# Kernel optimization log

Hardware: AMD Instinct MI355X
Metric: run time of the kernel (lower is better)

The kernel has to match this reference:

```python
import jax, jax.numpy as jnp
import numpy as np

B, POMO, N = 64, 200, 1000
EMB, H, D = 128, 8, 16  # head_num * qkv_dim == embedding_dim
SQRT_EMB = 11.313708498984761
CLIP = 10.0
LORA_SCALE = 16.0 / 16  # alpha / rank = 1.0


def setup_inputs() -> dict:
    key = jax.random.key(0)
    ks = jax.random.split(key, 12)
    s = 1.0 / np.sqrt(EMB)
    return {
        "encoded_nodes": jax.random.normal(ks[0], (B, N, EMB), jnp.float32),
        "encoded_q1": jax.random.normal(ks[1], (B, POMO, EMB), jnp.float32),
        "encoded_last_node": jax.random.normal(ks[2], (B, POMO, EMB), jnp.float32),
        "ninf_mask": jnp.zeros((B, POMO, N), jnp.float32),
        "Wq_first": jax.random.normal(ks[3], (H * D, EMB), jnp.float32) * s,
        "Wq_last": jax.random.normal(ks[4], (H * D, EMB), jnp.float32) * s,
        "Wk": jax.random.normal(ks[5], (H * D, EMB), jnp.float32) * s,
        "Wv": jax.random.normal(ks[6], (H * D, EMB), jnp.float32) * s,
        "Wcomb": jax.random.normal(ks[7], (EMB, H * D), jnp.float32) * s,
        "bcomb": jnp.zeros((EMB,), jnp.float32),
        "lora_q_A": jax.random.normal(ks[8], (16, EMB), jnp.float32) * s,
        "lora_q_B": jax.random.normal(ks[9], (H * D, 16), jnp.float32) * 0.01,
        "lora_c_A": jax.random.normal(ks[10], (16, H * D), jnp.float32) * s,
        "lora_c_B": jax.random.normal(ks[11], (EMB, 16), jnp.float32) * 0.01,
    }


def _heads(x):
    # [B, n, H*D] -> [B, H, n, D]
    b, n, _ = x.shape
    return x.reshape(b, n, H, D).transpose(0, 2, 1, 3)


def reference(encoded_nodes, encoded_q1, encoded_last_node, ninf_mask,
              Wq_first, Wq_last, Wk, Wv, Wcomb, bcomb,
              lora_q_A, lora_q_B, lora_c_A, lora_c_B):
    # set_kv
    k = _heads(encoded_nodes @ Wk.T)   # [B,H,N,D]
    v = _heads(encoded_nodes @ Wv.T)   # [B,H,N,D]
    # set_q1
    q_first = _heads(encoded_q1 @ Wq_first.T)  # [B,H,POMO,D]
    # forward: Wq_last + LoRA delta
    q_last_lin = encoded_last_node @ Wq_last.T \
        + ((encoded_last_node @ lora_q_A.T) @ lora_q_B.T) * LORA_SCALE
    q = q_first + _heads(q_last_lin)  # [B,H,POMO,D]
    # masked multi-head attention (rank3 mask broadcast over heads)
    score = jnp.einsum('bhnd,bhmd->bhnm', q, k) / jnp.sqrt(jnp.float32(D))
    score = score + ninf_mask[:, None, :, :]
    weights = jax.nn.softmax(score, axis=3)
    out = jnp.einsum('bhnm,bhmd->bhnd', weights, v)  # [B,H,POMO,D]
    out_concat = out.transpose(0, 2, 1, 3).reshape(encoded_q1.shape[0], -1, H * D)
    # combine + LoRA delta
    mh = out_concat @ Wcomb.T + bcomb \
        + ((out_concat @ lora_c_A.T) @ lora_c_B.T) * LORA_SCALE  # [B,POMO,EMB]
    # single-head scoring against encoder embeddings, tanh clip, mask, softmax
    score2 = jnp.einsum('bne,bme->bnm', mh, encoded_nodes) / SQRT_EMB
    score_masked = CLIP * jnp.tanh(score2) + ninf_mask
    probs = jax.nn.softmax(score_masked, axis=2)  # [B,POMO,N]
    return probs
```

## Files before the change

### kernel.cpp

```cpp
#include <hip/hip_runtime.h>
#include <hip/hip_bf16.h>


typedef _Float16 f16;
typedef _Float16 f16x2 __attribute__((ext_vector_type(2)));
typedef _Float16 f16x4 __attribute__((ext_vector_type(4)));
typedef _Float16 f16x8 __attribute__((ext_vector_type(8)));
typedef __fp16  h4   __attribute__((ext_vector_type(4)));
typedef float   f32x4 __attribute__((ext_vector_type(4)));

#define LORA_SCALE 1.0f

__device__ __forceinline__ f16x2 pk2(f16 a, f16 b){ f16x2 r; r[0]=a; r[1]=b; return r; }

#if __has_builtin(__builtin_amdgcn_fdot2)
__device__ __forceinline__ float fdot2f(f16x2 a, f16x2 b, float c){ return __builtin_amdgcn_fdot2(a, b, c, false); }
#else
__device__ __forceinline__ float fdot2f(f16x2 a, f16x2 b, float c){ return c + (float)a[0]*(float)b[0] + (float)a[1]*(float)b[1]; }
#endif

#if __has_builtin(__builtin_amdgcn_cvt_pkrtz)
__device__ __forceinline__ f16x2 pkrtz(float a, float b){
  return __builtin_bit_cast(f16x2, __builtin_amdgcn_cvt_pkrtz(a, b));
}
#else
__device__ __forceinline__ f16x2 pkrtz(float a, float b){ return pk2((f16)a, (f16)b); }
#endif

__device__ __forceinline__ f32x4 mfma16(f16x4 a, f16x4 b, f32x4 c){
  return __builtin_amdgcn_mfma_f32_16x16x16f16(
      __builtin_bit_cast(h4, a), __builtin_bit_cast(h4, b), c, 0, 0, 0);
}

__device__ __forceinline__ float sumsq16(const f16* p){
  const f16x8* v = (const f16x8*)p;
  f16x8 a = v[0], b = v[1];
  float s = 0.f;
  s = fdot2f(pk2(a[0],a[1]), pk2(a[0],a[1]), s);
  s = fdot2f(pk2(a[2],a[3]), pk2(a[2],a[3]), s);
  s = fdot2f(pk2(a[4],a[5]), pk2(a[4],a[5]), s);
  s = fdot2f(pk2(a[6],a[7]), pk2(a[6],a[7]), s);
  s = fdot2f(pk2(b[0],b[1]), pk2(b[0],b[1]), s);
  s = fdot2f(pk2(b[2],b[3]), pk2(b[2],b[3]), s);
  s = fdot2f(pk2(b[4],b[5]), pk2(b[4],b[5]), s);
  s = fdot2f(pk2(b[6],b[7]), pk2(b[6],b[7]), s);
  return s;
}

__global__ __launch_bounds__(256) void k0_wconv(const float* __restrict__ Wk,
    const float* __restrict__ Wv, f16* __restrict__ WkvF)
{
  const int i = blockIdx.x*256 + threadIdx.x;
  const float4 v = (i < 4096) ? ((const float4*)Wk)[i] : ((const float4*)Wv)[i-4096];
  f16x2 lo = pkrtz(v.x,v.y), hi = pkrtz(v.z,v.w);
  f16x4 o = __builtin_shufflevector(lo, hi, 0, 1, 2, 3);
  *(f16x4*)(WkvF + i*4) = o;
}

#define NSTR 132
#define WSTR 136
__global__ __launch_bounds__(256) void k1_proj(const float* __restrict__ nodes,
    const f16* __restrict__ WkvF,
    f16* __restrict__ nodesF, f16* __restrict__ Kp, f16* __restrict__ Vt)
{
  __shared__ f16 lds[64*NSTR];
  __shared__ f16 wlds[16*WSTR];
  const int tid = threadIdx.x, lane = tid & 63, w = tid >> 6;
  const int b = blockIdx.y;
  const int n0 = blockIdx.x * 64;
  const int rows = min(64, 1000 - n0);
  for (int i = tid; i < rows*32; i += 256) {
    const int r = i >> 5, cq = i & 31;
    float4 v = ((const float4*)(nodes + ((size_t)b*1000 + n0 + r)*128))[cq];
    f16x2 lo = pkrtz(v.x,v.y), hi = pkrtz(v.z,v.w);
    f16x4 o = __builtin_shufflevector(lo, hi, 0, 1, 2, 3);
    *(f16x4*)(lds + r*NSTR + cq*4) = o;
    *(f16x4*)(nodesF + ((size_t)b*1000 + n0 + r)*128 + cq*4) = o;
  }
  __syncthreads();
  const int col = lane & 15, g = lane >> 4, g4 = g*4;
  const int mloc = w*16 + col;
  f16x4 nf[8];
  #pragma unroll
  for (int kk = 0; kk < 8; ++kk)
    nf[kk] = *(const f16x4*)(lds + min(mloc, rows-1)*NSTR + kk*16 + g4);
  const int wr = tid >> 4, wc = tid & 15;
  for (int ct = 0; ct < 16; ++ct) {
    __syncthreads();
    *(f16x8*)(wlds + wr*WSTR + wc*8) =
        *(const f16x8*)(WkvF + (ct*16 + wr)*128 + wc*8);
    __syncthreads();
    f16x4 wf[8];
    #pragma unroll
    for (int kk = 0; kk < 8; ++kk)
      wf[kk] = *(const f16x4*)(wlds + col*WSTR + kk*16 + g4);
    f32x4 acc = {0.f, 0.f, 0.f, 0.f};
    if (ct < 8) {
      #pragma unroll
      for (int kk = 0; kk < 8; ++kk) acc = mfma16(wf[kk], nf[kk], acc);
      if (mloc < rows) {
        const int nn = n0 + mloc;
        f16x4 ov = __builtin_shufflevector(pk2((f16)acc[0],(f16)acc[1]),
                                           pk2((f16)acc[2],(f16)acc[3]), 0,1,2,3);
        *(f16x4*)(Kp + ((size_t)(b*8+ct)*1000 + nn)*16 + g4) = ov;
      }
    } else {
      #pragma unroll
      for (int kk = 0; kk < 8; ++kk) acc = mfma16(nf[kk], wf[kk], acc);
      if (w*16 + g4 + 3 < rows) {
        const int nbase = n0 + w*16 + g4;
        f16x4 ov = __builtin_shufflevector(pk2((f16)acc[0],(f16)acc[1]),
                                           pk2((f16)acc[2],(f16)acc[3]), 0,1,2,3);
        *(f16x4*)(Vt + ((size_t)(b*8+(ct-8))*16 + col)*1000 + nbase) = ov;
      }
    }
  }
}

__global__ __launch_bounds__(256) void k1b_kmax(const f16* __restrict__ Kp,
    float* __restrict__ kmaxA)
{
  __shared__ float wmax[4];
  const int bh = blockIdx.x, tid = threadIdx.x, lane = tid & 63, w = tid >> 6;
  const f16* base = Kp + (size_t)bh*16000;
  float mx = 0.f;
  for (int n = tid; n < 1000; n += 256) mx = fmaxf(mx, sumsq16(base + n*16));
  #pragma unroll
  for (int off = 32; off; off >>= 1) mx = fmaxf(mx, __shfl_xor(mx, off, 64));
  if (lane == 0) wmax[w] = mx;
  __syncthreads();
  if (tid == 0) {
    float m = fmaxf(fmaxf(wmax[0], wmax[1]), fmaxf(wmax[2], wmax[3]));
    kmaxA[bh] = sqrtf(m);
  }
}

__global__ __launch_bounds__(256) void k2_q(const float* __restrict__ q1,
    const float* __restrict__ last, const float* __restrict__ Wqf,
    const float* __restrict__ Wql, const float* __restrict__ lqA,
    const float* __restrict__ lqB, f16* __restrict__ qF)
{
  __shared__ f16 q1r[32*128];
  __shared__ f16 lar[32*128];
  __shared__ float t16[32*16];
  const int tid = threadIdx.x;
  const int row0 = blockIdx.x * 32;
  {
    const float4* s1 = (const float4*)(q1 + (size_t)row0*128);
    const float4* s2 = (const float4*)(last + (size_t)row0*128);
    f16x2* d1 = (f16x2*)q1r; f16x2* d2 = (f16x2*)lar;
    for (int i = tid; i < 32*32; i += 256) {
      float4 v = s1[i];
      d1[2*i] = pkrtz(v.x,v.y); d1[2*i+1] = pkrtz(v.z,v.w);
      float4 u = s2[i];
      d2[2*i] = pkrtz(u.x,u.y); d2[2*i+1] = pkrtz(u.z,u.w);
    }
  }
  __syncthreads();
  for (int idx = tid; idx < 32*16; idx += 256) {
    const int r = idx >> 4, kk = idx & 15;
    const f16x8* lrow = (const f16x8*)(lar + r*128);
    const float* arow = lqA + kk*128;
    float s = 0.f;
    #pragma unroll
    for (int cc = 0; cc < 16; ++cc) {
      f16x8 a = lrow[cc];
      float4 wa = *(const float4*)(arow + cc*8);
      float4 wb = *(const float4*)(arow + cc*8 + 4);
      s = fdot2f(pk2(a[0],a[1]), pkrtz(wa.x,wa.y), s);
      s = fdot2f(pk2(a[2],a[3]), pkrtz(wa.z,wa.w), s);
      s = fdot2f(pk2(a[4],a[5]), pkrtz(wb.x,wb.y), s);
      s = fdot2f(pk2(a[6],a[7]), pkrtz(wb.z,wb.w), s);
    }
    t16[idx] = s;
  }
  __syncthreads();
  const int c = tid & 127, rg = tid >> 7, rb = rg*16;
  float acc[16];
  #pragma unroll
  for (int r = 0; r < 16; ++r) acc[r] = 0.f;
  const float* wfr = Wqf + c*128;
  const float* wlr = Wql + c*128;
  for (int c0 = 0; c0 < 128; c0 += 16) {
    float4 f0 = *(const float4*)(wfr + c0);
    float4 f1 = *(const float4*)(wfr + c0 + 4);
    float4 f2 = *(const float4*)(wfr + c0 + 8);
    float4 f3 = *(const float4*)(wfr + c0 + 12);
    f16x2 wf[8] = { pkrtz(f0.x,f0.y), pkrtz(f0.z,f0.w), pkrtz(f1.x,f1.y), pkrtz(f1.z,f1.w),
                    pkrtz(f2.x,f2.y), pkrtz(f2.z,f2.w), pkrtz(f3.x,f3.y), pkrtz(f3.z,f3.w) };
    float4 g0 = *(const float4*)(wlr + c0);
    float4 g1 = *(const float4*)(wlr + c0 + 4);
    float4 g2 = *(const float4*)(wlr + c0 + 8);
    float4 g3 = *(const float4*)(wlr + c0 + 12);
    f16x2 wl[8] = { pkrtz(g0.x,g0.y), pkrtz(g0.z,g0.w), pkrtz(g1.x,g1.y), pkrtz(g1.z,g1.w),
                    pkrtz(g2.x,g2.y), pkrtz(g2.z,g2.w), pkrtz(g3.x,g3.y), pkrtz(g3.z,g3.w) };
    #pragma unroll
    for (int r = 0; r < 16; ++r) {
      const f16x8* qp = (const f16x8*)(q1r + (rb+r)*128 + c0);
      const f16x8* lp = (const f16x8*)(lar + (rb+r)*128 + c0);
      f16x8 a0 = qp[0], a1 = qp[1], b0 = lp[0], b1 = lp[1];
      float s = acc[r];
      s = fdot2f(pk2(a0[0],a0[1]), wf[0], s);
      s = fdot2f(pk2(a0[2],a0[3]), wf[1], s);
      s = fdot2f(pk2(a0[4],a0[5]), wf[2], s);
      s = fdot2f(pk2(a0[6],a0[7]), wf[3], s);
      s = fdot2f(pk2(a1[0],a1[1]), wf[4], s);
      s = fdot2f(pk2(a1[2],a1[3]), wf[5], s);
      s = fdot2f(pk2(a1[4],a1[5]), wf[6], s);
      s = fdot2f(pk2(a1[6],a1[7]), wf[7], s);
      s = fdot2f(pk2(b0[0],b0[1]), wl[0], s);
      s = fdot2f(pk2(b0[2],b0[3]), wl[1], s);
      s = fdot2f(pk2(b0[4],b0[5]), wl[2], s);
      s = fdot2f(pk2(b0[6],b0[7]), wl[3], s);
      s = fdot2f(pk2(b1[0],b1[1]), wl[4], s);
      s = fdot2f(pk2(b1[2],b1[3]), wl[5], s);
      s = fdot2f(pk2(b1[4],b1[5]), wl[6], s);
      s = fdot2f(pk2(b1[6],b1[7]), wl[7], s);
      acc[r] = s;
    }
  }
  const float* lb = lqB + c*16;
  float lbv[16];
  #pragma unroll
  for (int i = 0; i < 16; i += 4) {
    float4 t = *(const float4*)(lb + i);
    lbv[i] = t.x; lbv[i+1] = t.y; lbv[i+2] = t.z; lbv[i+3] = t.w;
  }
  #pragma unroll
  for (int r = 0; r < 16; ++r) {
    float dl = 0.f;
    #pragma unroll
    for (int kk = 0; kk < 16; ++kk) dl += t16[(rb+r)*16 + kk] * lbv[kk];
    acc[r] += dl * LORA_SCALE;
  }
  const int h = c >> 4, d = c & 15;
  #pragma unroll
  for (int r = 0; r < 16; ++r) {
    const int grow = row0 + rb + r;
    const int b = grow / 200, m = grow % 200;
    qF[(((size_t)b*8 + h)*200 + m)*16 + d] = (f16)acc[r];
  }
}

__global__ __launch_bounds__(256) void k2b_qnorm(const f16* __restrict__ qF,
    float* __restrict__ qnA)
{
  const int idx = blockIdx.x*256 + threadIdx.x;
  qnA[idx] = sqrtf(sumsq16(qF + (size_t)idx*16));
}

#define VSTRL 516
__global__ __launch_bounds__(512) void k3_attn(const f16* __restrict__ Kp,
    const f16* __restrict__ Vt, const f16* __restrict__ qF,
    const float* __restrict__ mask, const float* __restrict__ kmaxA,
    const float* __restrict__ qnA, f16* __restrict__ Opart,
    float* __restrict__ lpart)
{
  extern __shared__ char smem[];
  f16* Kl = (f16*)smem;
  f16* Vl = (f16*)(smem + 16384);
  const int tid = threadIdx.x;
  const int lane = tid & 63, w = tid >> 6;
  const int b = blockIdx.x, h = blockIdx.y, z = blockIdx.z;
  const int bh = b*8 + h;
  {
    const int nl = tid;
    const int n = z*512 + nl;
    f16x4 v0{}, v1{}, v2{}, v3{};
    if (n < 1000) {
      const f16x4* src = (const f16x4*)(Kp + (size_t)bh*16000 + n*16);
      v0 = src[0]; v1 = src[1]; v2 = src[2]; v3 = src[3];
    }
    const int sw = (nl >> 2) & 3;
    f16* dst = Kl + nl*16;
    *(f16x4*)(dst + (0^sw)*4) = v0;
    *(f16x4*)(dst + (1^sw)*4) = v1;
    *(f16x4*)(dst + (2^sw)*4) = v2;
    *(f16x4*)(dst + (3^sw)*4) = v3;
  }
  {
    const int d = tid >> 5, c16 = (tid & 31) * 16;
    const f16* srow = Vt + (size_t)bh*16000 + d*1000;
    f16* drow = Vl + d*VSTRL + c16;
    const int nbase = z*512 + c16;
    if (nbase + 15 < 1000) {
      const f16x4* s4 = (const f16x4*)(srow + nbase);
      *(f16x4*)(drow)    = s4[0];
      *(f16x4*)(drow+4)  = s4[1];
      *(f16x4*)(drow+8)  = s4[2];
      *(f16x4*)(drow+12) = s4[3];
    } else {
      for (int j = 0; j < 16; ++j) drow[j] = (nbase+j < 1000) ? srow[nbase+j] : (f16)0;
    }
  }
  __syncthreads();

  const int col = lane & 15, g = lane >> 4, g4 = g*4;
  const int kqoff = (g ^ (col >> 2)) * 4;
  const f32x4 zero = {0.f, 0.f, 0.f, 0.f};
  const int tA = w, tB = (w + 8 < 13) ? (w + 8) : 12;
  const int mA = tA*16, mB = tB*16;
  const int mqA = min(mA + col, 199), mqB = min(mB + col, 199);
  const f16x4 qfA = *(const f16x4*)(qF + (size_t)bh*3200 + mqA*16 + g4);
  const f16x4 qfB = *(const f16x4*)(qF + (size_t)bh*3200 + mqB*16 + g4);
  const float kmx = kmaxA[bh];
  const float mbA = -kmx * qnA[bh*200 + mqA] * 0.360673760f;
  const float mbB = -kmx * qnA[bh*200 + mqB] * 0.360673760f;
  const float* mpA = mask + ((size_t)b*200 + mqA)*1000 + z*512;
  const float* mpB = mask + ((size_t)b*200 + mqB)*1000 + z*512;

  f32x4 OA = zero, OB = zero;
  float lA0=0.f, lA1=0.f, lA2=0.f, lA3=0.f;
  float lB0=0.f, lB1=0.f, lB2=0.f, lB3=0.f;
  const int NTc = 32 - z*2;
  #pragma unroll 2
  for (int t = 0; t < NTc; ++t) {
    const int nl = t*16;
    const f16x4 kf = *(const f16x4*)(Kl + (nl+col)*16 + kqoff);
    f32x4 sA = mfma16(kf, qfA, zero);
    f32x4 sB = mfma16(kf, qfB, zero);
    const float4 mkA = *(const float4*)(mpA + nl + g4);
    const float4 mkB = *(const float4*)(mpB + nl + g4);
    const float pA0 = exp2f(fmaf(sA[0], 0.360673760f, fmaf(mkA.x, 1.44269504f, mbA)));
    const float pA1 = exp2f(fmaf(sA[1], 0.360673760f, fmaf(mkA.y, 1.44269504f, mbA)));
    const float pA2 = exp2f(fmaf(sA[2], 0.360673760f, fmaf(mkA.z, 1.44269504f, mbA)));
    const float pA3 = exp2f(fmaf(sA[3], 0.360673760f, fmaf(mkA.w, 1.44269504f, mbA)));
    const float pB0 = exp2f(fmaf(sB[0], 0.360673760f, fmaf(mkB.x, 1.44269504f, mbB)));
    const float pB1 = exp2f(fmaf(sB[1], 0.360673760f, fmaf(mkB.y, 1.44269504f, mbB)));
    const float pB2 = exp2f(fmaf(sB[2], 0.360673760f, fmaf(mkB.z, 1.44269504f, mbB)));
    const float pB3 = exp2f(fmaf(sB[3], 0.360673760f, fmaf(mkB.w, 1.44269504f, mbB)));
    lA0 += pA0; lA1 += pA1; lA2 += pA2; lA3 += pA3;
    lB0 += pB0; lB1 += pB1; lB2 += pB2; lB3 += pB3;
    const f16x4 pfA = __builtin_shufflevector(pkrtz(pA0,pA1), pkrtz(pA2,pA3), 0,1,2,3);
    const f16x4 pfB = __builtin_shufflevector(pkrtz(pB0,pB1), pkrtz(pB2,pB3), 0,1,2,3);
    const f16x4 vf = *(const f16x4*)(Vl + col*VSTRL + nl + g4);
    OA = mfma16(vf, pfA, OA);
    OB = mfma16(vf, pfB, OB);
  }
  if (z == 1) {
    const int nl = 480;
    const f16x4 kf = *(const f16x4*)(Kl + (nl+col)*16 + kqoff);
    f32x4 sA = mfma16(kf, qfA, zero);
    f32x4 sB = mfma16(kf, qfB, zero);
    float pA0=0.f,pA1=0.f,pA2=0.f,pA3=0.f, pB0=0.f,pB1=0.f,pB2=0.f,pB3=0.f;
    if (g < 2) {
      const float4 mkA = *(const float4*)(mpA + nl + g4);
      const float4 mkB = *(const float4*)(mpB + nl + g4);
      pA0 = exp2f(fmaf(sA[0], 0.360673760f, fmaf(mkA.x, 1.44269504f, mbA)));
      pA1 = exp2f(fmaf(sA[1], 0.360673760f, fmaf(mkA.y, 1.44269504f, mbA)));
      pA2 = exp2f(fmaf(sA[2], 0.360673760f, fmaf(mkA.z, 1.44269504f, mbA)));
      pA3 = exp2f(fmaf(sA[3], 0.360673760f, fmaf(mkA.w, 1.44269504f, mbA)));
      pB0 = exp2f(fmaf(sB[0], 0.360673760f, fmaf(mkB.x, 1.44269504f, mbB)));
      pB1 = exp2f(fmaf(sB[1], 0.360673760f, fmaf(mkB.y, 1.44269504f, mbB)));
      pB2 = exp2f(fmaf(sB[2], 0.360673760f, fmaf(mkB.z, 1.44269504f, mbB)));
      pB3 = exp2f(fmaf(sB[3], 0.360673760f, fmaf(mkB.w, 1.44269504f, mbB)));
      lA0 += pA0; lA1 += pA1; lA2 += pA2; lA3 += pA3;
      lB0 += pB0; lB1 += pB1; lB2 += pB2; lB3 += pB3;
    }
    const f16x4 pfA = __builtin_shufflevector(pkrtz(pA0,pA1), pkrtz(pA2,pA3), 0,1,2,3);
    const f16x4 pfB = __builtin_shufflevector(pkrtz(pB0,pB1), pkrtz(pB2,pB3), 0,1,2,3);
    const f16x4 vf = *(const f16x4*)(Vl + col*VSTRL + ((g < 2) ? (nl + g4) : 0));
    OA = mfma16(vf, pfA, OA);
    OB = mfma16(vf, pfB, OB);
  }
  float lA = (lA0 + lA1) + (lA2 + lA3);
  float lB = (lB0 + lB1) + (lB2 + lB3);
  lA += __shfl_xor(lA, 16, 64); lA += __shfl_xor(lA, 32, 64);
  lB += __shfl_xor(lB, 16, 64); lB += __shfl_xor(lB, 32, 64);
  const size_t pbase = (size_t)(z*512 + bh)*200;
  if (mA + col < 200) {
    const f16x4 ov = __builtin_shufflevector(pkrtz(OA[0], OA[1]), pkrtz(OA[2], OA[3]), 0,1,2,3);
    *(f16x4*)(Opart + (pbase + mA + col)*16 + g4) = ov;
    if (g == 0) lpart[pbase + mA + col] = lA;
  }
  if (mB + col < 200) {
    const f16x4 ov = __builtin_shufflevector(pkrtz(OB[0], OB[1]), pkrtz(OB[2], OB[3]), 0,1,2,3);
    *(f16x4*)(Opart + (pbase + mB + col)*16 + g4) = ov;
    if (g == 0) lpart[pbase + mB + col] = lB;
  }
}

__global__ __launch_bounds__(256) void k3c_comb(const f16* __restrict__ Opart,
    const float* __restrict__ lpart, f16* __restrict__ ocmh)
{
  const int idx = blockIdx.x*256 + threadIdx.x;
  const int r = idx >> 2, q = idx & 3;
  const f16x4 o0 = *(const f16x4*)(Opart + (size_t)r*16 + q*4);
  const f16x4 o1 = *(const f16x4*)(Opart + ((size_t)102400 + r)*16 + q*4);
  const float l = lpart[r] + lpart[102400 + r];
  const float inv = 1.f / fmaxf(l, 1e-35f);
  const int bh = r / 200, m = r - bh*200;
  const int b = bh >> 3, hh = bh & 7;
  const float v0 = ((float)o0[0] + (float)o1[0]) * inv;
  const float v1 = ((float)o0[1] + (float)o1[1]) * inv;
  const float v2 = ((float)o0[2] + (float)o1[2]) * inv;
  const float v3 = ((float)o0[3] + (float)o1[3]) * inv;
  const f16x4 o = __builtin_shufflevector(pkrtz(v0, v1), pkrtz(v2, v3), 0, 1, 2, 3);
  *(f16x4*)(ocmh + ((size_t)(b*200 + m)*128) + hh*16 + q*4) = o;
}

__global__ __launch_bounds__(256) void k4_comb(const f16* ocF,
    const float* __restrict__ Wc, const float* __restrict__ bc,
    const float* __restrict__ lcA, const float* __restrict__ lcB,
    f16* mhF)
{
  __shared__ f16 ocr[32*128];
  __shared__ float t16[32*16];
  const int tid = threadIdx.x;
  const int row0 = blockIdx.x * 32;
  {
    const f16x8* s1 = (const f16x8*)(ocF + (size_t)row0*128);
    f16x8* d1 = (f16x8*)ocr;
    for (int i = tid; i < 512; i += 256) d1[i] = s1[i];
  }
  __syncthreads();
  for (int idx = tid; idx < 32*16; idx += 256) {
    const int r = idx >> 4, kk = idx & 15;
    const f16x8* lrow = (const f16x8*)(ocr + r*128);
    const float* arow = lcA + kk*128;
    float s = 0.f;
    #pragma unroll
    for (int cc = 0; cc < 16; ++cc) {
      f16x8 a = lrow[cc];
      float4 wa = *(const float4*)(arow + cc*8);
      float4 wb = *(const float4*)(arow + cc*8 + 4);
      s = fdot2f(pk2(a[0],a[1]), pkrtz(wa.x,wa.y), s);
      s = fdot2f(pk2(a[2],a[3]), pkrtz(wa.z,wa.w), s);
      s = fdot2f(pk2(a[4],a[5]), pkrtz(wb.x,wb.y), s);
      s = fdot2f(pk2(a[6],a[7]), pkrtz(wb.z,wb.w), s);
    }
    t16[idx] = s;
  }
  __syncthreads();
  const int c = tid & 127, rg = tid >> 7, rb = rg*16;
  float acc[16];
  const float bias = bc[c];
  #pragma unroll
  for (int r = 0; r < 16; ++r) acc[r] = bias;
  const float* wrow = Wc + c*128;
  for (int c0 = 0; c0 < 128; c0 += 16) {
    float4 w0 = *(const float4*)(wrow + c0);
    float4 w1 = *(const float4*)(wrow + c0 + 4);
    float4 w2 = *(const float4*)(wrow + c0 + 8);
    float4 w3 = *(const float4*)(wrow + c0 + 12);
    f16x2 wv[8] = { pkrtz(w0.x,w0.y), pkrtz(w0.z,w0.w), pkrtz(w1.x,w1.y), pkrtz(w1.z,w1.w),
                    pkrtz(w2.x,w2.y), pkrtz(w2.z,w2.w), pkrtz(w3.x,w3.y), pkrtz(w3.z,w3.w) };
    #pragma unroll
    for (int r = 0; r < 16; ++r) {
      const f16x8* op = (const f16x8*)(ocr + (rb+r)*128 + c0);
      f16x8 a0 = op[0], a1 = op[1];
      float s = acc[r];
      s = fdot2f(pk2(a0[0],a0[1]), wv[0], s);
      s = fdot2f(pk2(a0[2],a0[3]), wv[1], s);
      s = fdot2f(pk2(a0[4],a0[5]), wv[2], s);
      s = fdot2f(pk2(a0[6],a0[7]), wv[3], s);
      s = fdot2f(pk2(a1[0],a1[1]), wv[4], s);
      s = fdot2f(pk2(a1[2],a1[3]), wv[5], s);
      s = fdot2f(pk2(a1[4],a1[5]), wv[6], s);
      s = fdot2f(pk2(a1[6],a1[7]), wv[7], s);
      acc[r] = s;
    }
  }
  const float* lb = lcB + c*16;
  float lbv[16];
  #pragma unroll
  for (int i = 0; i < 16; i += 4) {
    float4 t = *(const float4*)(lb + i);
    lbv[i] = t.x; lbv[i+1] = t.y; lbv[i+2] = t.z; lbv[i+3] = t.w;
  }
  #pragma unroll
  for (int r = 0; r < 16; ++r) {
    float dl = 0.f;
    #pragma unroll
    for (int kk = 0; kk < 16; ++kk) dl += t16[(rb+r)*16 + kk] * lbv[kk];
    acc[r] += dl * LORA_SCALE;
  }
  #pragma unroll
  for (int r = 0; r < 16; ++r) {
    mhF[(size_t)(row0 + rb + r)*128 + c] = (f16)acc[r];
  }
}

__global__ __launch_bounds__(1024) void k5_final(const f16* __restrict__ mhF,
    const f16* __restrict__ nodesF, const float* __restrict__ mask,
    float* __restrict__ out)
{
  __shared__ float sumsA[16][16];
  __shared__ float sumsB[16][16];
  const int tid = threadIdx.x, lane = tid & 63, w = tid >> 6;
  const int b = blockIdx.x, j = blockIdx.y;
  const int col = lane & 15, g = lane >> 4, g4 = g*4;
  const int tmA = 2*j, tmB = min(2*j + 1, 12);
  const int mA = tmA*16 + col, mB = tmB*16 + col;
  const int mqA = min(mA, 199), mqB = min(mB, 199);
  f16x4 bfA[8], bfB[8];
  {
    const f16* a = mhF + (size_t)(b*200 + mqA)*128;
    const f16* bb = mhF + (size_t)(b*200 + mqB)*128;
    #pragma unroll
    for (int kk = 0; kk < 8; ++kk) {
      bfA[kk] = *(const f16x4*)(a + kk*16 + g4);
      bfB[kk] = *(const f16x4*)(bb + kk*16 + g4);
    }
  }
  const float* mrowA = mask + (size_t)(b*200 + mqA)*1000;
  const float* mrowB = mask + (size_t)(b*200 + mqB)*1000;
  const f16* nb = nodesF + (size_t)b*128000;
  f16x4 pfA[4], pfB[4];
  float lsumA = 0.f, lsumB = 0.f;
  #pragma unroll
  for (int i = 0; i < 4; ++i) {
    const int t = w + i*16;
    float pA0 = 0.f, pA1 = 0.f, pA2 = 0.f, pA3 = 0.f;
    float pB0 = 0.f, pB1 = 0.f, pB2 = 0.f, pB3 = 0.f;
    if (t < 63) {
      const int nr = min(t*16 + col, 999);
      const f16* na = nb + nr*128;
      f32x4 accA = {0.f, 0.f, 0.f, 0.f};
      f32x4 accB = {0.f, 0.f, 0.f, 0.f};
      #pragma unroll
      for (int kk = 0; kk < 8; ++kk) {
        f16x4 af = *(const f16x4*)(na + kk*16 + g4);
        accA = mfma16(af, bfA[kk], accA);
        accB = mfma16(af, bfB[kk], accB);
      }
      const int n0 = t*16 + g4;
      float mkvA[4] = {0.f, 0.f, 0.f, 0.f};
      float mkvB[4] = {0.f, 0.f, 0.f, 0.f};
      if (n0 + 3 < 1000) {
        float4 mkA = *(const float4*)(mrowA + n0);
        float4 mkB = *(const float4*)(mrowB + n0);
        mkvA[0] = mkA.x; mkvA[1] = mkA.y; mkvA[2] = mkA.z; mkvA[3] = mkA.w;
        mkvB[0] = mkB.x; mkvB[1] = mkB.y; mkvB[2] = mkB.z; mkvB[3] = mkB.w;
      }
      float pvA[4], pvB[4];
      #pragma unroll
      for (int r = 0; r < 4; ++r) {
        const bool ok = (n0 + r < 1000);
        float xA = accA[r] * 0.08838834764831845f;
        float eA = exp2f(xA * 2.8853900817779268f);
        float thA = 1.f - 2.f/(eA + 1.f);
        float tA0 = exp2f((10.f*thA + mkvA[r]) * 1.44269504f);
        pvA[r] = ok ? tA0 : 0.f;
        lsumA += pvA[r];
        float xB = accB[r] * 0.08838834764831845f;
        float eB = exp2f(xB * 2.8853900817779268f);
        float thB = 1.f - 2.f/(eB + 1.f);
        float tB0 = exp2f((10.f*thB + mkvB[r]) * 1.44269504f);
        pvB[r] = ok ? tB0 : 0.f;
        lsumB += pvB[r];
      }
      pA0 = pvA[0]; pA1 = pvA[1]; pA2 = pvA[2]; pA3 = pvA[3];
      pB0 = pvB[0]; pB1 = pvB[1]; pB2 = pvB[2]; pB3 = pvB[3];
    }
    pfA[i] = __builtin_shufflevector(pkrtz(pA0, pA1), pkrtz(pA2, pA3), 0, 1, 2, 3);
    pfB[i] = __builtin_shufflevector(pkrtz(pB0, pB1), pkrtz(pB2, pB3), 0, 1, 2, 3);
  }
  lsumA += __shfl_xor(lsumA, 16, 64);
  lsumA += __shfl_xor(lsumA, 32, 64);
  lsumB += __shfl_xor(lsumB, 16, 64);
  lsumB += __shfl_xor(lsumB, 32, 64);
  if (lane < 16) { sumsA[w][lane] = lsumA; sumsB[w][lane] = lsumB; }
  __syncthreads();
  float SA = 0.f, SB = 0.f;
  #pragma unroll
  for (int ww = 0; ww < 16; ++ww) { SA += sumsA[ww][col]; SB += sumsB[ww][col]; }
  const float invA = 1.f / SA;
  const float invB = 1.f / SB;
  if (mA < 200) {
    float* ob = out + (size_t)(b*200 + mA)*1000;
    #pragma unroll
    for (int i = 0; i < 4; ++i) {
      const int t = w + i*16;
      if (t < 63) {
        const int n0 = t*16 + g4;
        const f16x4 pv = pfA[i];
        if (n0 + 3 < 1000) {
          float4 o;
          o.x = (float)pv[0]*invA; o.y = (float)pv[1]*invA;
          o.z = (float)pv[2]*invA; o.w = (float)pv[3]*invA;
          *(float4*)(ob + n0) = o;
        } else {
          #pragma unroll
          for (int r = 0; r < 4; ++r) if (n0 + r < 1000) ob[n0+r] = (float)pv[r]*invA;
        }
      }
    }
  }
  if (mB < 200 && tmB != tmA) {
    float* ob = out + (size_t)(b*200 + mB)*1000;
    #pragma unroll
    for (int i = 0; i < 4; ++i) {
      const int t = w + i*16;
      if (t < 63) {
        const int n0 = t*16 + g4;
        const f16x4 pv = pfB[i];
        if (n0 + 3 < 1000) {
          float4 o;
          o.x = (float)pv[0]*invB; o.y = (float)pv[1]*invB;
          o.z = (float)pv[2]*invB; o.w = (float)pv[3]*invB;
          *(float4*)(ob + n0) = o;
        } else {
          #pragma unroll
          for (int r = 0; r < 4; ++r) if (n0 + r < 1000) ob[n0+r] = (float)pv[r]*invB;
        }
      }
    }
  }
}

extern "C" void kernel_launch(void* const* d_in, const int* in_sizes, int n_in,
                              void* d_out, int out_size, void* d_ws, size_t ws_size,
                              hipStream_t stream)
{
  (void)in_sizes; (void)n_in; (void)out_size; (void)ws_size;
  const float* nodes = (const float*)d_in[0];
  const float* q1    = (const float*)d_in[1];
  const float* last  = (const float*)d_in[2];
  const float* mask  = (const float*)d_in[3];
  const float* Wqf   = (const float*)d_in[4];
  const float* Wql   = (const float*)d_in[5];
  const float* Wk    = (const float*)d_in[6];
  const float* Wv    = (const float*)d_in[7];
  const float* Wc    = (const float*)d_in[8];
  const float* bc    = (const float*)d_in[9];
  const float* lqA   = (const float*)d_in[10];
  const float* lqB   = (const float*)d_in[11];
  const float* lcA   = (const float*)d_in[12];
  const float* lcB   = (const float*)d_in[13];
  float* out = (float*)d_out;
  char* ws = (char*)d_ws;
  f16* nodesF  = (f16*)(ws);
  f16* Kp      = (f16*)(ws + 16384000);
  f16* Vt      = (f16*)(ws + 32768000);
  f16* qF      = (f16*)(ws + 49152000);
  f16* ocmh    = (f16*)(ws + 52428800);
  f16* WkvF    = (f16*)(ws + 55705600);
  float* kmaxA = (float*)(ws + 55771136);
  float* qnA   = (float*)(ws + 55773184);
  f16* OpartF  = (f16*)(ws + 56182784);
  float* lpart = (float*)(ws + 62736384);

  k0_wconv<<<dim3(32), 256, 0, stream>>>(Wk, Wv, WkvF);
  k1_proj<<<dim3(16, 64), 256, 0, stream>>>(nodes, WkvF, nodesF, Kp, Vt);
  k1b_kmax<<<dim3(512), 256, 0, stream>>>(Kp, kmaxA);
  k2_q<<<dim3(400), 256, 0, stream>>>(q1, last, Wqf, Wql, lqA, lqB, qF);
  k2b_qnorm<<<dim3(400), 256, 0, stream>>>(qF, qnA);
  k3_attn<<<dim3(64, 8, 2), 512, 32896, stream>>>(Kp, Vt, qF, mask, kmaxA, qnA, OpartF, lpart);
  k3c_comb<<<dim3(1600), 256, 0, stream>>>(OpartF, lpart, ocmh);
  k4_comb<<<dim3(400), 256, 0, stream>>>(ocmh, Wc, bc, lcA, lcB, ocmh);
  k5_final<<<dim3(64, 7), 1024, 0, stream>>>(ocmh, nodesF, mask, out);
}
```

Measured before the change: 206.9 us.

## Pre-tile mask into fp16 MFMA-fragment layout shared by attention and final kernels

Adds a preprocessing kernel that converts the fp32 mask into fp16, pre-scaled by log2(e), stored in the exact per-lane fragment order used by the attention and final-scoring kernels. Both consumers then read contiguous half-size tiles instead of strided fp32 rows, with 8 attention heads re-reading the same mask. The mask is still read once in full fp32 by the new kernel, and fp16 rounding of mask values (including -inf) is a precision risk. The path is enabled only when the workspace is large enough.

```diff
diff --git a/kernel.cpp b/kernel.cpp
--- a/kernel.cpp
+++ b/kernel.cpp
@@ -10,6 +10,7 @@
 typedef float   f32x4 __attribute__((ext_vector_type(4)));
 
 #define LORA_SCALE 1.0f
+#define L2E 1.44269504f
 
 __device__ __forceinline__ f16x2 pk2(f16 a, f16 b){ f16x2 r; r[0]=a; r[1]=b; return r; }
 
@@ -55,6 +56,22 @@
   f16x2 lo = pkrtz(v.x,v.y), hi = pkrtz(v.z,v.w);
   f16x4 o = __builtin_shufflevector(lo, hi, 0, 1, 2, 3);
   *(f16x4*)(WkvF + i*4) = o;
+}
+
+__global__ __launch_bounds__(256) void kpre_mtile(const float* __restrict__ mask,
+    f16* __restrict__ maskT)
+{
+  const int tid = threadIdx.x, lane = tid & 63, w = tid >> 6;
+  const int b = blockIdx.x, mt = blockIdx.y;
+  const int t = blockIdx.z*4 + w;
+  if (t >= 63) return;
+  const int col = lane & 15, g = lane >> 4;
+  const int row = min(mt*16 + col, 199);
+  const int n0 = t*16 + g*4;
+  float4 v = {0.f, 0.f, 0.f, 0.f};
+  if (n0 + 3 < 1000) v = *(const float4*)(mask + ((size_t)b*200 + row)*1000 + n0);
+  f16x4 o = __builtin_shufflevector(pkrtz(v.x*L2E, v.y*L2E), pkrtz(v.z*L2E, v.w*L2E), 0,1,2,3);
+  *(f16x4*)(maskT + (((size_t)(b*13 + mt)*63) + t)*256 + lane*4) = o;
 }
 
 #define NSTR 132
@@ -250,11 +267,12 @@
 }
 
 #define VSTRL 516
+template<int TILED>
 __global__ __launch_bounds__(512) void k3_attn(const f16* __restrict__ Kp,
     const f16* __restrict__ Vt, const f16* __restrict__ qF,
-    const float* __restrict__ mask, const float* __restrict__ kmaxA,
-    const float* __restrict__ qnA, f16* __restrict__ Opart,
-    float* __restrict__ lpart)
+    const float* __restrict__ mask, const f16* __restrict__ maskT,
+    const float* __restrict__ kmaxA, const float* __restrict__ qnA,
+    f16* __restrict__ Opart, float* __restrict__ lpart)
 {
   extern __shared__ char smem[];
   f16* Kl = (f16*)smem;
@@ -308,6 +326,8 @@
   const float mbB = -kmx * qnA[bh*200 + mqB] * 0.360673760f;
   const float* mpA = mask + ((size_t)b*200 + mqA)*1000 + z*512;
   const float* mpB = mask + ((size_t)b*200 + mqB)*1000 + z*512;
+  const f16* mtA = maskT + ((size_t)(b*13 + tA)*63)*256 + lane*4;
+  const f16* mtB = maskT + ((size_t)(b*13 + tB)*63)*256 + lane*4;
 
   f32x4 OA = zero, OB = zero;
   float lA0=0.f, lA1=0.f, lA2=0.f, lA3=0.f;
@@ -316,19 +336,34 @@
   #pragma unroll 2
   for (int t = 0; t < NTc; ++t) {
     const int nl = t*16;
+    const int tg = z*32 + t;
     const f16x4 kf = *(const f16x4*)(Kl + (nl+col)*16 + kqoff);
     f32x4 sA = mfma16(kf, qfA, zero);
     f32x4 sB = mfma16(kf, qfB, zero);
-    const float4 mkA = *(const float4*)(mpA + nl + g4);
-    const float4 mkB = *(const float4*)(mpB + nl + g4);
-    const float pA0 = exp2f(fmaf(sA[0], 0.360673760f, fmaf(mkA.x, 1.44269504f, mbA)));
-    const float pA1 = exp2f(fmaf(sA[1], 0.360673760f, fmaf(mkA.y, 1.44269504f, mbA)));
-    const float pA2 = exp2f(fmaf(sA[2], 0.360673760f, fmaf(mkA.z, 1.44269504f, mbA)));
-    const float pA3 = exp2f(fmaf(sA[3], 0.360673760f, fmaf(mkA.w, 1.44269504f, mbA)));
-    const float pB0 = exp2f(fmaf(sB[0], 0.360673760f, fmaf(mkB.x, 1.44269504f, mbB)));
-    const float pB1 = exp2f(fmaf(sB[1], 0.360673760f, fmaf(mkB.y, 1.44269504f, mbB)));
-    const float pB2 = exp2f(fmaf(sB[2], 0.360673760f, fmaf(mkB.z, 1.44269504f, mbB)));
-    const float pB3 = exp2f(fmaf(sB[3], 0.360673760f, fmaf(mkB.w, 1.44269504f, mbB)));
+    float xA0, xA1, xA2, xA3, xB0, xB1, xB2, xB3;
+    if (TILED) {
+      const f16x4 ka = *(const f16x4*)(mtA + tg*256);
+      const f16x4 kb = *(const f16x4*)(mtB + tg*256);
+      xA0 = (float)ka[0] + mbA; xA1 = (float)ka[1] + mbA;
+      xA2 = (float)ka[2] + mbA; xA3 = (float)ka[3] + mbA;
+      xB0 = (float)kb[0] + mbB; xB1 = (float)kb[1] + mbB;
+      xB2 = (float)kb[2] + mbB; xB3 = (float)kb[3] + mbB;
+    } else {
+      const float4 mkA = *(const float4*)(mpA + nl + g4);
+      const float4 mkB = *(const float4*)(mpB + nl + g4);
+      xA0 = fmaf(mkA.x, L2E, mbA); xA1 = fmaf(mkA.y, L2E, mbA);
+      xA2 = fmaf(mkA.z, L2E, mbA); xA3 = fmaf(mkA.w, L2E, mbA);
+      xB0 = fmaf(mkB.x, L2E, mbB); xB1 = fmaf(mkB.y, L2E, mbB);
+      xB2 = fmaf(mkB.z, L2E, mbB); xB3 = fmaf(mkB.w, L2E, mbB);
+    }
+    const float pA0 = exp2f(fmaf(sA[0], 0.360673760f, xA0));
+    const float pA1 = exp2f(fmaf(sA[1], 0.360673760f, xA1));
+    const float pA2 = exp2f(fmaf(sA[2], 0.360673760f, xA2));
+    const float pA3 = exp2f(fmaf(sA[3], 0.360673760f, xA3));
+    const float pB0 = exp2f(fmaf(sB[0], 0.360673760f, xB0));
+    const float pB1 = exp2f(fmaf(sB[1], 0.360673760f, xB1));
+    const float pB2 = exp2f(fmaf(sB[2], 0.360673760f, xB2));
+    const float pB3 = exp2f(fmaf(sB[3], 0.360673760f, xB3));
     lA0 += pA0; lA1 += pA1; lA2 += pA2; lA3 += pA3;
     lB0 += pB0; lB1 += pB1; lB2 += pB2; lB3 += pB3;
     const f16x4 pfA = __builtin_shufflevector(pkrtz(pA0,pA1), pkrtz(pA2,pA3), 0,1,2,3);
@@ -344,16 +379,30 @@
     f32x4 sB = mfma16(kf, qfB, zero);
     float pA0=0.f,pA1=0.f,pA2=0.f,pA3=0.f, pB0=0.f,pB1=0.f,pB2=0.f,pB3=0.f;
     if (g < 2) {
-      const float4 mkA = *(const float4*)(mpA + nl + g4);
-      const float4 mkB = *(const float4*)(mpB + nl + g4);
-      pA0 = exp2f(fmaf(sA[0], 0.360673760f, fmaf(mkA.x, 1.44269504f, mbA)));
-      pA1 = exp2f(fmaf(sA[1], 0.360673760f, fmaf(mkA.y, 1.44269504f, mbA)));
-      pA2 = exp2f(fmaf(sA[2], 0.360673760f, fmaf(mkA.z, 1.44269504f, mbA)));
-      pA3 = exp2f(fmaf(sA[3], 0.360673760f, fmaf(mkA.w, 1.44269504f, mbA)));
-      pB0 = exp2f(fmaf(sB[0], 0.360673760f, fmaf(mkB.x, 1.44269504f, mbB)));
-      pB1 = exp2f(fmaf(sB[1], 0.360673760f, fmaf(mkB.y, 1.44269504f, mbB)));
-      pB2 = exp2f(fmaf(sB[2], 0.360673760f, fmaf(mkB.z, 1.44269504f, mbB)));
-      pB3 = exp2f(fmaf(sB[3], 0.360673760f, fmaf(mkB.w, 1.44269504f, mbB)));
+      float xA0, xA1, xA2, xA3, xB0, xB1, xB2, xB3;
+      if (TILED) {
+        const f16x4 ka = *(const f16x4*)(mtA + 62*256);
+        const f16x4 kb = *(const f16x4*)(mtB + 62*256);
+        xA0 = (float)ka[0] + mbA; xA1 = (float)ka[1] + mbA;
+        xA2 = (float)ka[2] + mbA; xA3 = (float)ka[3] + mbA;
+        xB0 = (float)kb[0] + mbB; xB1 = (float)kb[1] + mbB;
+        xB2 = (float)kb[2] + mbB; xB3 = (float)kb[3] + mbB;
+      } else {
+        const float4 mkA = *(const float4*)(mpA + nl + g4);
+        const float4 mkB = *(const float4*)(mpB + nl + g4);
+        xA0 = fmaf(mkA.x, L2E, mbA); xA1 = fmaf(mkA.y, L2E, mbA);
+        xA2 = fmaf(mkA.z, L2E, mbA); xA3 = fmaf(mkA.w, L2E, mbA);
+        xB0 = fmaf(mkB.x, L2E, mbB); xB1 = fmaf(mkB.y, L2E, mbB);
+        xB2 = fmaf(mkB.z, L2E, mbB); xB3 = fmaf(mkB.w, L2E, mbB);
+      }
+      pA0 = exp2f(fmaf(sA[0], 0.360673760f, xA0));
+      pA1 = exp2f(fmaf(sA[1], 0.360673760f, xA1));
+      pA2 = exp2f(fmaf(sA[2], 0.360673760f, xA2));
+      pA3 = exp2f(fmaf(sA[3], 0.360673760f, xA3));
+      pB0 = exp2f(fmaf(sB[0], 0.360673760f, xB0));
+      pB1 = exp2f(fmaf(sB[1], 0.360673760f, xB1));
+      pB2 = exp2f(fmaf(sB[2], 0.360673760f, xB2));
+      pB3 = exp2f(fmaf(sB[3], 0.360673760f, xB3));
       lA0 += pA0; lA1 += pA1; lA2 += pA2; lA3 += pA3;
       lB0 += pB0; lB1 += pB1; lB2 += pB2; lB3 += pB3;
     }
@@ -481,9 +530,10 @@
   }
 }
 
+template<int TILED>
 __global__ __launch_bounds__(1024) void k5_final(const f16* __restrict__ mhF,
     const f16* __restrict__ nodesF, const float* __restrict__ mask,
-    float* __restrict__ out)
+    const f16* __restrict__ maskT, float* __restrict__ out)
 {
   __shared__ float sumsA[16][16];
   __shared__ float sumsB[16][16];
@@ -505,6 +555,8 @@
   }
   const float* mrowA = mask + (size_t)(b*200 + mqA)*1000;
   const float* mrowB = mask + (size_t)(b*200 + mqB)*1000;
+  const f16* mtA = maskT + ((size_t)(b*13 + tmA)*63)*256 + lane*4;
+  const f16* mtB = maskT + ((size_t)(b*13 + tmB)*63)*256 + lane*4;
   const f16* nb = nodesF + (size_t)b*128000;
   f16x4 pfA[4], pfB[4];
   float lsumA = 0.f, lsumB = 0.f;
@@ -525,13 +577,17 @@
         accB = mfma16(af, bfB[kk], accB);
       }
       const int n0 = t*16 + g4;
-      float mkvA[4] = {0.f, 0.f, 0.f, 0.f};
-      float mkvB[4] = {0.f, 0.f, 0.f, 0.f};
-      if (n0 + 3 < 1000) {
-        float4 mkA = *(const float4*)(mrowA + n0);
-        float4 mkB = *(const float4*)(mrowB + n0);
-        mkvA[0] = mkA.x; mkvA[1] = mkA.y; mkvA[2] = mkA.z; mkvA[3] = mkA.w;
-        mkvB[0] = mkB.x; mkvB[1] = mkB.y; mkvB[2] = mkB.z; mkvB[3] = mkB.w;
+      float mklA[4], mklB[4];
+      if (TILED) {
+        const f16x4 ka = *(const f16x4*)(mtA + t*256);
+        const f16x4 kb = *(const f16x4*)(mtB + t*256);
+        #pragma unroll
+        for (int r = 0; r < 4; ++r) { mklA[r] = (float)ka[r]; mklB[r] = (float)kb[r]; }
+      } else {
+        float4 a = {0,0,0,0}, bb = {0,0,0,0};
+        if (n0 + 3 < 1000) { a = *(const float4*)(mrowA + n0); bb = *(const float4*)(mrowB + n0); }
+        mklA[0]=a.x*L2E; mklA[1]=a.y*L2E; mklA[2]=a.z*L2E; mklA[3]=a.w*L2E;
+        mklB[0]=bb.x*L2E; mklB[1]=bb.y*L2E; mklB[2]=bb.z*L2E; mklB[3]=bb.w*L2E;
       }
       float pvA[4], pvB[4];
       #pragma unroll
@@ -540,13 +596,13 @@
         float xA = accA[r] * 0.08838834764831845f;
         float eA = exp2f(xA * 2.8853900817779268f);
         float thA = 1.f - 2.f/(eA + 1.f);
-        float tA0 = exp2f((10.f*thA + mkvA[r]) * 1.44269504f);
+        float tA0 = exp2f(fmaf(thA, 14.4269504f, mklA[r]));
         pvA[r] = ok ? tA0 : 0.f;
         lsumA += pvA[r];
         float xB = accB[r] * 0.08838834764831845f;
         float eB = exp2f(xB * 2.8853900817779268f);
         float thB = 1.f - 2.f/(eB + 1.f);
-        float tB0 = exp2f((10.f*thB + mkvB[r]) * 1.44269504f);
+        float tB0 = exp2f(fmaf(thB, 14.4269504f, mklB[r]));
         pvB[r] = ok ? tB0 : 0.f;
         lsumB += pvB[r];
       }
@@ -613,7 +669,7 @@
                               void* d_out, int out_size, void* d_ws, size_t ws_size,
                               hipStream_t stream)
 {
-  (void)in_sizes; (void)n_in; (void)out_size; (void)ws_size;
+  (void)in_sizes; (void)n_in; (void)out_size;
   const float* nodes = (const float*)d_in[0];
   const float* q1    = (const float*)d_in[1];
   const float* last  = (const float*)d_in[2];
@@ -640,14 +696,23 @@
   float* qnA   = (float*)(ws + 55773184);
   f16* OpartF  = (f16*)(ws + 56182784);
   float* lpart = (float*)(ws + 62736384);
+  f16* maskT   = (f16*)(ws + 63555584);
+  const bool tiled = ws_size >= 90392576ULL;
 
   k0_wconv<<<dim3(32), 256, 0, stream>>>(Wk, Wv, WkvF);
+  if (tiled) kpre_mtile<<<dim3(64, 13, 16), 256, 0, stream>>>(mask, maskT);
   k1_proj<<<dim3(16, 64), 256, 0, stream>>>(nodes, WkvF, nodesF, Kp, Vt);
   k1b_kmax<<<dim3(512), 256, 0, stream>>>(Kp, kmaxA);
   k2_q<<<dim3(400), 256, 0, stream>>>(q1, last, Wqf, Wql, lqA, lqB, qF);
   k2b_qnorm<<<dim3(400), 256, 0, stream>>>(qF, qnA);
-  k3_attn<<<dim3(64, 8, 2), 512, 32896, stream>>>(Kp, Vt, qF, mask, kmaxA, qnA, OpartF, lpart);
+  if (tiled)
+    k3_attn<1><<<dim3(64, 8, 2), 512, 32896, stream>>>(Kp, Vt, qF, mask, maskT, kmaxA, qnA, OpartF, lpart);
+  else
+    k3_attn<0><<<dim3(64, 8, 2), 512, 32896, stream>>>(Kp, Vt, qF, mask, maskT, kmaxA, qnA, OpartF, lpart);
   k3c_comb<<<dim3(1600), 256, 0, stream>>>(OpartF, lpart, ocmh);
   k4_comb<<<dim3(400), 256, 0, stream>>>(ocmh, Wc, bc, lcA, lcB, ocmh);
-  k5_final<<<dim3(64, 7), 1024, 0, stream>>>(ocmh, nodesF, mask, out);
-}
+  if (tiled)
+    k5_final<1><<<dim3(64, 7), 1024, 0, stream>>>(ocmh, nodesF, mask, maskT, out);
+  else
+    k5_final<0><<<dim3(64, 7), 1024, 0, stream>>>(ocmh, nodesF, mask, maskT, out);
+}
```

Measured after the change: 220.7 us. 6.7% more time.

## Store nodes in MFMA-fragment order and stage final output through LDS

Applied to the files above, without the earlier changes.

k1_proj now writes the fp16 node copy in a tiled layout that matches the MFMA A-fragment order, padding the last tile by replicating row 999. k5_final can then load each fragment with one contiguous 8-byte read per lane instead of strided row reads. The output probabilities are staged in a 16x1012 float LDS buffer so each row is written to global memory with fully coalesced per-thread stores rather than scattered float4 writes. The trade-off is about 64KB of LDS per block, which may lower occupancy, extra barriers, and a slightly larger workspace.

```diff
diff --git a/kernel.cpp b/kernel.cpp
--- a/kernel.cpp
+++ b/kernel.cpp
@@ -10,6 +10,7 @@
 typedef float   f32x4 __attribute__((ext_vector_type(4)));
 
 #define LORA_SCALE 1.0f
+#define L2E 1.44269504f
 
 __device__ __forceinline__ f16x2 pk2(f16 a, f16 b){ f16x2 r; r[0]=a; r[1]=b; return r; }
 
@@ -61,7 +62,7 @@
 #define WSTR 136
 __global__ __launch_bounds__(256) void k1_proj(const float* __restrict__ nodes,
     const f16* __restrict__ WkvF,
-    f16* __restrict__ nodesF, f16* __restrict__ Kp, f16* __restrict__ Vt)
+    f16* __restrict__ nodesT, f16* __restrict__ Kp, f16* __restrict__ Vt)
 {
   __shared__ f16 lds[64*NSTR];
   __shared__ f16 wlds[16*WSTR];
@@ -75,7 +76,16 @@
     f16x2 lo = pkrtz(v.x,v.y), hi = pkrtz(v.z,v.w);
     f16x4 o = __builtin_shufflevector(lo, hi, 0, 1, 2, 3);
     *(f16x4*)(lds + r*NSTR + cq*4) = o;
-    *(f16x4*)(nodesF + ((size_t)b*1000 + n0 + r)*128 + cq*4) = o;
+    const int grow = n0 + r;
+    const int t = grow >> 4, gcol = grow & 15;
+    const int kk = cq >> 2, gg = cq & 3;
+    f16* dstT = nodesT + (((size_t)(b*63 + t)*8 + kk)*256);
+    *(f16x4*)(dstT + (gg*16 + gcol)*4) = o;
+    if (grow == 999) {
+      f16* d62 = nodesT + (((size_t)(b*63 + 62)*8 + kk)*256);
+      #pragma unroll
+      for (int cf = 8; cf < 16; ++cf) *(f16x4*)(d62 + (gg*16 + cf)*4) = o;
+    }
   }
   __syncthreads();
   const int col = lane & 15, g = lane >> 4, g4 = g*4;
@@ -321,14 +331,14 @@
     f32x4 sB = mfma16(kf, qfB, zero);
     const float4 mkA = *(const float4*)(mpA + nl + g4);
     const float4 mkB = *(const float4*)(mpB + nl + g4);
-    const float pA0 = exp2f(fmaf(sA[0], 0.360673760f, fmaf(mkA.x, 1.44269504f, mbA)));
-    const float pA1 = exp2f(fmaf(sA[1], 0.360673760f, fmaf(mkA.y, 1.44269504f, mbA)));
-    const float pA2 = exp2f(fmaf(sA[2], 0.360673760f, fmaf(mkA.z, 1.44269504f, mbA)));
-    const float pA3 = exp2f(fmaf(sA[3], 0.360673760f, fmaf(mkA.w, 1.44269504f, mbA)));
-    const float pB0 = exp2f(fmaf(sB[0], 0.360673760f, fmaf(mkB.x, 1.44269504f, mbB)));
-    const float pB1 = exp2f(fmaf(sB[1], 0.360673760f, fmaf(mkB.y, 1.44269504f, mbB)));
-    const float pB2 = exp2f(fmaf(sB[2], 0.360673760f, fmaf(mkB.z, 1.44269504f, mbB)));
-    const float pB3 = exp2f(fmaf(sB[3], 0.360673760f, fmaf(mkB.w, 1.44269504f, mbB)));
+    const float pA0 = exp2f(fmaf(sA[0], 0.360673760f, fmaf(mkA.x, L2E, mbA)));
+    const float pA1 = exp2f(fmaf(sA[1], 0.360673760f, fmaf(mkA.y, L2E, mbA)));
+    const float pA2 = exp2f(fmaf(sA[2], 0.360673760f, fmaf(mkA.z, L2E, mbA)));
+    const float pA3 = exp2f(fmaf(sA[3], 0.360673760f, fmaf(mkA.w, L2E, mbA)));
+    const float pB0 = exp2f(fmaf(sB[0], 0.360673760f, fmaf(mkB.x, L2E, mbB)));
+    const float pB1 = exp2f(fmaf(sB[1], 0.360673760f, fmaf(mkB.y, L2E, mbB)));
+    const float pB2 = exp2f(fmaf(sB[2], 0.360673760f, fmaf(mkB.z, L2E, mbB)));
+    const float pB3 = exp2f(fmaf(sB[3], 0.360673760f, fmaf(mkB.w, L2E, mbB)));
     lA0 += pA0; lA1 += pA1; lA2 += pA2; lA3 += pA3;
     lB0 += pB0; lB1 += pB1; lB2 += pB2; lB3 += pB3;
     const f16x4 pfA = __builtin_shufflevector(pkrtz(pA0,pA1), pkrtz(pA2,pA3), 0,1,2,3);
@@ -346,14 +356,14 @@
     if (g < 2) {
       const float4 mkA = *(const float4*)(mpA + nl + g4);
       const float4 mkB = *(const float4*)(mpB + nl + g4);
-      pA0 = exp2f(fmaf(sA[0], 0.360673760f, fmaf(mkA.x, 1.44269504f, mbA)));
-      pA1 = exp2f(fmaf(sA[1], 0.360673760f, fmaf(mkA.y, 1.44269504f, mbA)));
-      pA2 = exp2f(fmaf(sA[2], 0.360673760f, fmaf(mkA.z, 1.44269504f, mbA)));
-      pA3 = exp2f(fmaf(sA[3], 0.360673760f, fmaf(mkA.w, 1.44269504f, mbA)));
-      pB0 = exp2f(fmaf(sB[0], 0.360673760f, fmaf(mkB.x, 1.44269504f, mbB)));
-      pB1 = exp2f(fmaf(sB[1], 0.360673760f, fmaf(mkB.y, 1.44269504f, mbB)));
-      pB2 = exp2f(fmaf(sB[2], 0.360673760f, fmaf(mkB.z, 1.44269504f, mbB)));
-      pB3 = exp2f(fmaf(sB[3], 0.360673760f, fmaf(mkB.w, 1.44269504f, mbB)));
+      pA0 = exp2f(fmaf(sA[0], 0.360673760f, fmaf(mkA.x, L2E, mbA)));
+      pA1 = exp2f(fmaf(sA[1], 0.360673760f, fmaf(mkA.y, L2E, mbA)));
+      pA2 = exp2f(fmaf(sA[2], 0.360673760f, fmaf(mkA.z, L2E, mbA)));
+      pA3 = exp2f(fmaf(sA[3], 0.360673760f, fmaf(mkA.w, L2E, mbA)));
+      pB0 = exp2f(fmaf(sB[0], 0.360673760f, fmaf(mkB.x, L2E, mbB)));
+      pB1 = exp2f(fmaf(sB[1], 0.360673760f, fmaf(mkB.y, L2E, mbB)));
+      pB2 = exp2f(fmaf(sB[2], 0.360673760f, fmaf(mkB.z, L2E, mbB)));
+      pB3 = exp2f(fmaf(sB[3], 0.360673760f, fmaf(mkB.w, L2E, mbB)));
       lA0 += pA0; lA1 += pA1; lA2 += pA2; lA3 += pA3;
       lB0 += pB0; lB1 += pB1; lB2 += pB2; lB3 += pB3;
     }
@@ -482,11 +492,12 @@
 }
 
 __global__ __launch_bounds__(1024) void k5_final(const f16* __restrict__ mhF,
-    const f16* __restrict__ nodesF, const float* __restrict__ mask,
+    const f16* __restrict__ nodesT, const float* __restrict__ mask,
     float* __restrict__ out)
 {
   __shared__ float sumsA[16][16];
   __shared__ float sumsB[16][16];
+  __shared__ float obuf[16][1012];
   const int tid = threadIdx.x, lane = tid & 63, w = tid >> 6;
   const int b = blockIdx.x, j = blockIdx.y;
   const int col = lane & 15, g = lane >> 4, g4 = g*4;
@@ -505,7 +516,7 @@
   }
   const float* mrowA = mask + (size_t)(b*200 + mqA)*1000;
   const float* mrowB = mask + (size_t)(b*200 + mqB)*1000;
-  const f16* nb = nodesF + (size_t)b*128000;
+  const f16* ntb = nodesT + (size_t)b*129024;
   f16x4 pfA[4], pfB[4];
   float lsumA = 0.f, lsumB = 0.f;
   #pragma unroll
@@ -514,13 +525,12 @@
     float pA0 = 0.f, pA1 = 0.f, pA2 = 0.f, pA3 = 0.f;
     float pB0 = 0.f, pB1 = 0.f, pB2 = 0.f, pB3 = 0.f;
     if (t < 63) {
-      const int nr = min(t*16 + col, 999);
-      const f16* na = nb + nr*128;
+      const f16* na = ntb + (size_t)t*2048;
       f32x4 accA = {0.f, 0.f, 0.f, 0.f};
       f32x4 accB = {0.f, 0.f, 0.f, 0.f};
       #pragma unroll
       for (int kk = 0; kk < 8; ++kk) {
-        f16x4 af = *(const f16x4*)(na + kk*16 + g4);
+        f16x4 af = *(const f16x4*)(na + kk*256 + lane*4);
         accA = mfma16(af, bfA[kk], accA);
         accB = mfma16(af, bfB[kk], accB);
       }
@@ -540,13 +550,13 @@
         float xA = accA[r] * 0.08838834764831845f;
         float eA = exp2f(xA * 2.8853900817779268f);
         float thA = 1.f - 2.f/(eA + 1.f);
-        float tA0 = exp2f((10.f*thA + mkvA[r]) * 1.44269504f);
+        float tA0 = exp2f((10.f*thA + mkvA[r]) * L2E);
         pvA[r] = ok ? tA0 : 0.f;
         lsumA += pvA[r];
         float xB = accB[r] * 0.08838834764831845f;
         float eB = exp2f(xB * 2.8853900817779268f);
         float thB = 1.f - 2.f/(eB + 1.f);
-        float tB0 = exp2f((10.f*thB + mkvB[r]) * 1.44269504f);
+        float tB0 = exp2f((10.f*thB + mkvB[r]) * L2E);
         pvB[r] = ok ? tB0 : 0.f;
         lsumB += pvB[r];
       }
@@ -567,43 +577,40 @@
   for (int ww = 0; ww < 16; ++ww) { SA += sumsA[ww][col]; SB += sumsB[ww][col]; }
   const float invA = 1.f / SA;
   const float invB = 1.f / SB;
-  if (mA < 200) {
-    float* ob = out + (size_t)(b*200 + mA)*1000;
+  #pragma unroll
+  for (int i = 0; i < 4; ++i) {
+    const int t = w + i*16;
+    if (t < 63) {
+      const f16x4 pv = pfA[i];
+      const int n0 = t*16 + g4;
+      #pragma unroll
+      for (int r = 0; r < 4; ++r) obuf[col][n0 + r] = (float)pv[r]*invA;
+    }
+  }
+  __syncthreads();
+  if (tid < 1000) {
+    for (int rr = 0; rr < 16; ++rr) {
+      const int m = tmA*16 + rr;
+      if (m < 200) out[((size_t)b*200 + m)*1000 + tid] = obuf[rr][tid];
+    }
+  }
+  __syncthreads();
+  if (tmB != tmA) {
     #pragma unroll
     for (int i = 0; i < 4; ++i) {
       const int t = w + i*16;
       if (t < 63) {
+        const f16x4 pv = pfB[i];
         const int n0 = t*16 + g4;
-        const f16x4 pv = pfA[i];
-        if (n0 + 3 < 1000) {
-          float4 o;
-          o.x = (float)pv[0]*invA; o.y = (float)pv[1]*invA;
-          o.z = (float)pv[2]*invA; o.w = (float)pv[3]*invA;
-          *(float4*)(ob + n0) = o;
-        } else {
-          #pragma unroll
-          for (int r = 0; r < 4; ++r) if (n0 + r < 1000) ob[n0+r] = (float)pv[r]*invA;
-        }
+        #pragma unroll
+        for (int r = 0; r < 4; ++r) obuf[col][n0 + r] = (float)pv[r]*invB;
       }
     }
-  }
-  if (mB < 200 && tmB != tmA) {
-    float* ob = out + (size_t)(b*200 + mB)*1000;
-    #pragma unroll
-    for (int i = 0; i < 4; ++i) {
-      const int t = w + i*16;
-      if (t < 63) {
-        const int n0 = t*16 + g4;
-        const f16x4 pv = pfB[i];
-        if (n0 + 3 < 1000) {
-          float4 o;
-          o.x = (float)pv[0]*invB; o.y = (float)pv[1]*invB;
-          o.z = (float)pv[2]*invB; o.w = (float)pv[3]*invB;
-          *(float4*)(ob + n0) = o;
-        } else {
-          #pragma unroll
-          for (int r = 0; r < 4; ++r) if (n0 + r < 1000) ob[n0+r] = (float)pv[r]*invB;
-        }
+    __syncthreads();
+    if (tid < 1000) {
+      for (int rr = 0; rr < 16; ++rr) {
+        const int m = tmB*16 + rr;
+        if (m < 200) out[((size_t)b*200 + m)*1000 + tid] = obuf[rr][tid];
       }
     }
   }
@@ -630,7 +637,6 @@
   const float* lcB   = (const float*)d_in[13];
   float* out = (float*)d_out;
   char* ws = (char*)d_ws;
-  f16* nodesF  = (f16*)(ws);
   f16* Kp      = (f16*)(ws + 16384000);
   f16* Vt      = (f16*)(ws + 32768000);
   f16* qF      = (f16*)(ws + 49152000);
@@ -640,14 +646,15 @@
   float* qnA   = (float*)(ws + 55773184);
   f16* OpartF  = (f16*)(ws + 56182784);
   float* lpart = (float*)(ws + 62736384);
+  f16* nodesT  = (f16*)(ws + 63555584);
 
   k0_wconv<<<dim3(32), 256, 0, stream>>>(Wk, Wv, WkvF);
-  k1_proj<<<dim3(16, 64), 256, 0, stream>>>(nodes, WkvF, nodesF, Kp, Vt);
+  k1_proj<<<dim3(16, 64), 256, 0, stream>>>(nodes, WkvF, nodesT, Kp, Vt);
   k1b_kmax<<<dim3(512), 256, 0, stream>>>(Kp, kmaxA);
   k2_q<<<dim3(400), 256, 0, stream>>>(q1, last, Wqf, Wql, lqA, lqB, qF);
   k2b_qnorm<<<dim3(400), 256, 0, stream>>>(qF, qnA);
   k3_attn<<<dim3(64, 8, 2), 512, 32896, stream>>>(Kp, Vt, qF, mask, kmaxA, qnA, OpartF, lpart);
   k3c_comb<<<dim3(1600), 256, 0, stream>>>(OpartF, lpart, ocmh);
   k4_comb<<<dim3(400), 256, 0, stream>>>(ocmh, Wc, bc, lcA, lcB, ocmh);
-  k5_final<<<dim3(64, 7), 1024, 0, stream>>>(ocmh, nodesF, mask, out);
-}
+  k5_final<<<dim3(64, 7), 1024, 0, stream>>>(ocmh, nodesT, mask, out);
+}
```

Result: faster. 195.4 us (-5.5%).
